# Optimization experiments

Hardware: AMD Instinct MI355X
Metric: run time of the kernel (lower is better)

Reference implementation:

```python
import jax, jax.numpy as jnp
import numpy as np

N = 50000   # total_ent
R = 16      # total_rel
D = 64      # emb_dim
F_IN = 128  # feat_in
L = 2       # gcn_layers
E = 100000  # edges per relation
EPS = 1e-12


def setup_inputs() -> dict:
    key = jax.random.key(0)
    ks = jax.random.split(key, 6)
    x = jax.random.normal(ks[0], (N, F_IN), jnp.float32)
    # xavier-uniform-ish scaled params
    ent_emb = jax.random.normal(ks[1], (F_IN, D), jnp.float32) * (1.0 / np.sqrt(F_IN))
    rel_trans = jax.random.normal(ks[2], (L, R, D, D), jnp.float32) * (1.0 / np.sqrt(D))
    edge_row = jax.random.randint(ks[3], (R, E), 0, N)
    edge_col = jax.random.randint(ks[4], (R, E), 0, N)
    edge_val = jax.random.uniform(ks[5], (R, E), jnp.float32)
    return dict(x=x, ent_emb=ent_emb, rel_trans=rel_trans,
                edge_row=edge_row, edge_col=edge_col, edge_val=edge_val)


def reference(x, ent_emb, rel_trans, edge_row, edge_col, edge_val):
    # emb = x @ ent_emb : [N, D]
    emb = x @ ent_emb

    def spmm_per_rel(emb):
        # per-relation sparse.mm: out[r, row] += val * emb[col]
        def one_rel(row, col, val):
            return jax.ops.segment_sum(val[:, None] * emb[col], row, num_segments=N)
        return jax.vmap(one_rel)(edge_row, edge_col, edge_val)  # [R, N, D]

    for l in range(L):
        emb_acc = spmm_per_rel(emb)                             # [R, N, D]
        # tmp[r] = (W_r @ emb_acc[r]^T)^T = emb_acc[r] @ W_r^T
        tmp = jnp.einsum('rne,rde->rnd', emb_acc, rel_trans[l])  # [R, N, D]
        emb = jax.nn.relu(tmp.sum(axis=0))                       # [N, D]

    # F.normalize(emb) : L2 over dim=1 with eps clamp
    norm = jnp.linalg.norm(emb, axis=1, keepdims=True)
    return emb / jnp.maximum(norm, EPS)
```

## Files before the change

### kernel.cpp

```cpp
#include <hip/hip_runtime.h>

#define Nn 50000
#define Rr 16
#define Dd 64
#define Fin 128
#define Ee 100000
#define NE (Rr * Ee)
#define NBKT 782
#define CB 256
#define EPB (NE / CB)
#define SCTOT (NBKT * CB)
#define SC_NB (SCTOT / 256)
#define NTILE (Nn / 16)

typedef __attribute__((ext_vector_type(8))) short short8;
typedef __attribute__((ext_vector_type(4))) float f32x4;
typedef unsigned short ushort_t;

__device__ inline ushort_t f2bf(float x) {
  union { float f; unsigned u; } v; v.f = x;
  unsigned u = v.u;
  return (ushort_t)((u + 0x7FFFu + ((u >> 16) & 1u)) >> 16);
}
__device__ inline float bf2f(ushort_t h) {
  union { unsigned u; float f; } v; v.u = ((unsigned)h) << 16; return v.f;
}

#define INIT_TILES 3125
#define INIT_NB 782
#define CONVW_NB 512
__global__ __launch_bounds__(256) void pre_k(const float* __restrict__ x,
                                             const float* __restrict__ ent,
                                             ushort_t* __restrict__ emb0,
                                             const float* __restrict__ rel,
                                             ushort_t* __restrict__ wbf,
                                             const int* __restrict__ erow,
                                             int* __restrict__ cnt) {
  __shared__ int lh[NBKT];
  int b = blockIdx.x;
  if (b < INIT_NB) {
    int wave = threadIdx.x >> 6, lane = threadIdx.x & 63;
    int nt = lane & 15, quad = lane >> 4;
    int tile = b * 4 + wave;
    if (tile >= INIT_TILES) return;
    const float* xr = x + ((long)tile * 16 + nt) * Fin + quad * 8;
    short8 afrag[4];
#pragma unroll
    for (int ks = 0; ks < 4; ++ks) {
      float4 p0 = *(const float4*)(xr + ks * 32);
      float4 p1 = *(const float4*)(xr + ks * 32 + 4);
      short8 a;
      a[0] = (short)f2bf(p0.x); a[1] = (short)f2bf(p0.y);
      a[2] = (short)f2bf(p0.z); a[3] = (short)f2bf(p0.w);
      a[4] = (short)f2bf(p1.x); a[5] = (short)f2bf(p1.y);
      a[6] = (short)f2bf(p1.z); a[7] = (short)f2bf(p1.w);
      afrag[ks] = a;
    }
    f32x4 acc[4];
#pragma unroll
    for (int dt = 0; dt < 4; ++dt) acc[dt] = (f32x4){0.f, 0.f, 0.f, 0.f};
#pragma unroll
    for (int ks = 0; ks < 4; ++ks) {
#pragma unroll
      for (int dt = 0; dt < 4; ++dt) {
        short8 bfr;
#pragma unroll
        for (int j = 0; j < 8; ++j)
          bfr[j] = (short)f2bf(ent[(unsigned)(ks * 32 + quad * 8 + j) * Dd + dt * 16 + nt]);
        acc[dt] = __builtin_amdgcn_mfma_f32_16x16x32_bf16(afrag[ks], bfr, acc[dt], 0, 0, 0);
      }
    }
#pragma unroll
    for (int dt = 0; dt < 4; ++dt)
#pragma unroll
      for (int reg = 0; reg < 4; ++reg) {
        int row = tile * 16 + quad * 4 + reg;
        emb0[(unsigned)row * Dd + dt * 16 + nt] = f2bf(acc[dt][reg]);
      }
  } else if (b < INIT_NB + CONVW_NB) {
    int i = (b - INIT_NB) * 256 + threadIdx.x;
    wbf[i] = f2bf(rel[i]);
  } else {
    int blk = b - INIT_NB - CONVW_NB;
    int t = threadIdx.x;
    for (int i = t; i < NBKT; i += 256) lh[i] = 0;
    __syncthreads();
    int r = blk >> 4;
    long gbase = (long)r * Ee + (blk & 15) * EPB;
    for (int i = t; i < EPB; i += 256)
      atomicAdd(&lh[erow[gbase + i] >> 6], 1);
    __syncthreads();
    for (int i = t; i < NBKT; i += 256) cnt[i * CB + blk] = lh[i];
  }
}

__global__ __launch_bounds__(256) void scan1_k(const int* __restrict__ cnt,
                                               int* __restrict__ bsum) {
  __shared__ int ls[256];
  int t = threadIdx.x;
  ls[t] = cnt[blockIdx.x * 256 + t];
  __syncthreads();
  for (int off = 128; off >= 1; off >>= 1) {
    if (t < off) ls[t] += ls[t + off];
    __syncthreads();
  }
  if (t == 0) bsum[blockIdx.x] = ls[0];
}

__global__ __launch_bounds__(1024) void scan2_k(int* __restrict__ bsum) {
  __shared__ int ls[1024];
  int t = threadIdx.x;
  int v = (t < SC_NB) ? bsum[t] : 0;
  ls[t] = v;
  __syncthreads();
  for (int off = 1; off < 1024; off <<= 1) {
    int x = (t >= off) ? ls[t - off] : 0;
    __syncthreads();
    ls[t] += x;
    __syncthreads();
  }
  if (t < SC_NB) bsum[t] = ls[t] - v;
}

__global__ __launch_bounds__(256) void scan3_k(int* __restrict__ cnt,
                                               const int* __restrict__ bsum,
                                               int* __restrict__ cbase,
                                               int* __restrict__ offs) {
  __shared__ int ls[256];
  int t = threadIdx.x, i = blockIdx.x * 256 + t;
  int v = cnt[i];
  ls[t] = v;
  __syncthreads();
  for (int off = 1; off < 256; off <<= 1) {
    int x = (t >= off) ? ls[t - off] : 0;
    __syncthreads();
    ls[t] += x;
    __syncthreads();
  }
  int excl = ls[t] - v + bsum[blockIdx.x];
  cnt[i] = excl;
  if (t == 0) cbase[blockIdx.x] = excl;
  if (i == SCTOT - 1) { cbase[NBKT] = NE; offs[Nn] = NE; }
}

__global__ __launch_bounds__(256) void place_k(const int* __restrict__ erow,
                                               const int* __restrict__ ecol,
                                               const float* __restrict__ ev,
                                               const int* __restrict__ base,
                                               uint2* __restrict__ ebkt) {
  __shared__ int lofs[NBKT];
  int blk = blockIdx.x, t = threadIdx.x;
  for (int i = t; i < NBKT; i += 256) lofs[i] = base[i * CB + blk];
  __syncthreads();
  int r = blk >> 4;
  long gbase = (long)r * Ee + (blk & 15) * EPB;
  for (int i = t; i < EPB; i += 256) {
    long idx = gbase + i;
    int row = erow[idx];
    int pos = atomicAdd(&lofs[row >> 6], 1);
    unsigned vb = f2bf(ev[idx]);
    ebkt[pos] = make_uint2(((unsigned)(row & 63) << 4) | (unsigned)r,
                           (vb << 16) | (unsigned)ecol[idx]);
  }
}

__global__ __launch_bounds__(256) void csort_k(const uint2* __restrict__ ebkt,
                                               const int* __restrict__ cbase,
                                               uint2* __restrict__ ed2,
                                               int* __restrict__ offs) {
  __shared__ int lcnt[64], lstart[64], lcur[64];
  int c = blockIdx.x, t = threadIdx.x;
  int s = cbase[c], e = cbase[c + 1];
  if (t < 64) lcnt[t] = 0;
  __syncthreads();
  for (int i = s + t; i < e; i += 256) atomicAdd(&lcnt[ebkt[i].x >> 4], 1);
  __syncthreads();
  if (t == 0) {
    int run = 0;
    for (int rl = 0; rl < 64; ++rl) {
      int cc = lcnt[rl];
      lstart[rl] = run; lcur[rl] = run; run += cc;
    }
  }
  __syncthreads();
  int nrow = Nn - c * 64; if (nrow > 64) nrow = 64;
  if (t < nrow) offs[c * 64 + t] = s + lstart[t];
  for (int i = s + t; i < e; i += 256) {
    uint2 q = ebkt[i];
    int pos = s + atomicAdd(&lcur[q.x >> 4], 1);
    ed2[pos] = make_uint2(q.x & 15u, q.y);
  }
}

__global__ __launch_bounds__(256) void fused_k(const ushort_t* __restrict__ emb,
                                               const int* __restrict__ offs,
                                               const uint2* __restrict__ ed2,
                                               const ushort_t* __restrict__ wl,
                                               ushort_t* __restrict__ embout,
                                               float* __restrict__ finout,
                                               int fin) {
  __shared__ ushort_t Zt[16 * 1024];
  __shared__ f32x4 ssred[4][4];
  const int lane = threadIdx.x & 63;
  const int wave = threadIdx.x >> 6;
  const int nt = lane & 15, quad = lane >> 4;
  const int tile = blockIdx.x;

  const int qb = quad << 3;
  const ushort_t* embnt = emb + nt;
  char* ztb = (char*)Zt;
  union AW { unsigned w[4]; short8 v; };

  for (int rr = 0; rr < 4; ++rr) {
    const int rl = wave * 4 + rr;
    const int row = tile * 16 + rl;
    int off_l = (lane < 2) ? offs[row + lane] : 0;
    const int base = __shfl(off_l, 0, 64);
    const int len  = __shfl(off_l, 1, 64) - base;

    f32x4 acc[4];
#pragma unroll
    for (int dt = 0; dt < 4; ++dt) acc[dt] = (f32x4){0.f, 0.f, 0.f, 0.f};

    for (int c = 0; c < len; c += 32) {
      int p = c + (lane & 31);
      uint2 myed = (p < len) ? ed2[base + p] : make_uint2(0u, 0u);

      unsigned yw[4][4];
      unsigned aw[4];
#pragma unroll
      for (int jp = 0; jp < 4; ++jp) {
        unsigned q0 = (unsigned)__shfl((int)myed.y, qb + 2 * jp, 64);
        unsigned q1 = (unsigned)__shfl((int)myed.y, qb + 2 * jp + 1, 64);
        unsigned x0 = (unsigned)__shfl((int)myed.x, qb + 2 * jp, 64);
        unsigned x1 = (unsigned)__shfl((int)myed.x, qb + 2 * jp + 1, 64);
        const ushort_t* e0 = embnt + (q0 & 0xFFFFu) * 64u;
        const ushort_t* e1 = embnt + (q1 & 0xFFFFu) * 64u;
#pragma unroll
        for (int dt = 0; dt < 4; ++dt)
          yw[dt][jp] = (unsigned)e0[dt * 16] | ((unsigned)e1[dt * 16] << 16);
        unsigned t0 = (x0 == (unsigned)nt) ? (q0 >> 16) : 0u;
        unsigned t1 = (x1 == (unsigned)nt) ? (q1 >> 16) : 0u;
        aw[jp] = t0 | (t1 << 16);
      }

      AW af;
      af.w[0] = aw[0]; af.w[1] = aw[1]; af.w[2] = aw[2]; af.w[3] = aw[3];
#pragma unroll
      for (int dt = 0; dt < 4; ++dt) {
        AW bf;
#pragma unroll
        for (int jp = 0; jp < 4; ++jp) bf.w[jp] = yw[dt][jp];
        acc[dt] = __builtin_amdgcn_mfma_f32_16x16x32_bf16(af.v, bf.v, acc[dt], 0, 0, 0);
      }
    }

    const unsigned swz = (unsigned)((rl & 7) << 4);
    const unsigned rb = (unsigned)(rl * 2048 + quad * 512);
#pragma unroll
    for (int dt = 0; dt < 4; ++dt)
#pragma unroll
      for (int reg = 0; reg < 4; ++reg) {
        unsigned hv = (unsigned)f2bf(acc[dt][reg]);
        unsigned pv = (unsigned)__shfl_xor((int)hv, 1, 64);
        if ((nt & 1) == 0) {
          unsigned lg = rb + (unsigned)(reg * 128 + dt * 32 + nt * 2);
          *(unsigned*)(ztb + (lg ^ swz)) = hv | (pv << 16);
        }
      }
  }
  __syncthreads();

  const int s0 = nt * 2048 + (((quad    ) ^ (nt & 7)) << 4);
  const int s1 = nt * 2048 + (((quad + 4) ^ (nt & 7)) << 4);
  f32x4 accA = (f32x4){0.f, 0.f, 0.f, 0.f};
  f32x4 accB = (f32x4){0.f, 0.f, 0.f, 0.f};
#pragma unroll
  for (int r = 0; r < 16; r += 2) {
    const char* ab0 = ztb + r * 128;
    const char* ab1 = ztb + (r + 1) * 128;
    short8 a00 = *(const short8*)(ab0 + s0);
    short8 a01 = *(const short8*)(ab0 + s1);
    short8 a10 = *(const short8*)(ab1 + s0);
    short8 a11 = *(const short8*)(ab1 + s1);
    const ushort_t* bp0 = wl + (unsigned)(r * Dd + wave * 16 + nt) * Dd + qb;
    const ushort_t* bp1 = wl + (unsigned)((r + 1) * Dd + wave * 16 + nt) * Dd + qb;
    short8 b00 = *(const short8*)(bp0);
    short8 b01 = *(const short8*)(bp0 + 32);
    short8 b10 = *(const short8*)(bp1);
    short8 b11 = *(const short8*)(bp1 + 32);
    accA = __builtin_amdgcn_mfma_f32_16x16x32_bf16(a00, b00, accA, 0, 0, 0);
    accA = __builtin_amdgcn_mfma_f32_16x16x32_bf16(a01, b01, accA, 0, 0, 0);
    accB = __builtin_amdgcn_mfma_f32_16x16x32_bf16(a10, b10, accB, 0, 0, 0);
    accB = __builtin_amdgcn_mfma_f32_16x16x32_bf16(a11, b11, accB, 0, 0, 0);
  }
  f32x4 accO;
#pragma unroll
  for (int reg = 0; reg < 4; ++reg) accO[reg] = accA[reg] + accB[reg];

  if (!fin) {
#pragma unroll
    for (int reg = 0; reg < 4; ++reg) {
      int row = tile * 16 + quad * 4 + reg;
      embout[(unsigned)row * 64u + wave * 16 + nt] = f2bf(fmaxf(accO[reg], 0.f));
    }
  } else {
    float v[4];
    f32x4 ssq;
#pragma unroll
    for (int reg = 0; reg < 4; ++reg) {
      v[reg] = fmaxf(accO[reg], 0.f);
      ssq[reg] = v[reg] * v[reg];
    }
#pragma unroll
    for (int off = 8; off >= 1; off >>= 1)
#pragma unroll
      for (int reg = 0; reg < 4; ++reg)
        ssq[reg] += __shfl_xor(ssq[reg], off, 64);
    if (nt == 0) ssred[wave][quad] = ssq;
    __syncthreads();
    f32x4 t0 = ssred[0][quad], t1 = ssred[1][quad];
    f32x4 t2 = ssred[2][quad], t3 = ssred[3][quad];
#pragma unroll
    for (int reg = 0; reg < 4; ++reg) {
      float tot = t0[reg] + t1[reg] + t2[reg] + t3[reg];
      float sc = 1.f / fmaxf(sqrtf(tot), 1e-12f);
      int row = tile * 16 + quad * 4 + reg;
      finout[(unsigned)row * 64u + wave * 16 + nt] = v[reg] * sc;
    }
  }
}

extern "C" void kernel_launch(void* const* d_in, const int* in_sizes, int n_in,
                              void* d_out, int out_size, void* d_ws, size_t ws_size,
                              hipStream_t stream) {
  const float* x   = (const float*)d_in[0];
  const float* ent = (const float*)d_in[1];
  const float* rel = (const float*)d_in[2];
  const int* erow  = (const int*)d_in[3];
  const int* ecol  = (const int*)d_in[4];
  const float* ev  = (const float*)d_in[5];
  float* out = (float*)d_out;

  char* p = (char*)d_ws;
  ushort_t* emb_a = (ushort_t*)p;  p += (size_t)Nn * Dd * 2;
  ushort_t* emb_b = (ushort_t*)p;  p += (size_t)Nn * Dd * 2;
  ushort_t* wbf   = (ushort_t*)p;  p += (size_t)2 * Rr * Dd * Dd * 2;
  uint2* ebkt     = (uint2*)p;     p += (size_t)NE * 8;
  uint2* ed2      = (uint2*)p;     p += (size_t)NE * 8;
  int* cnt        = (int*)p;       p += (size_t)SCTOT * 4;
  int* bsum       = (int*)p;       p += (size_t)(SC_NB + 8) * 4;
  int* cbase      = (int*)p;       p += (size_t)(NBKT + 8) * 4;
  int* offs       = (int*)p;       p += (size_t)(Nn + 8) * 4;

  pre_k<<<INIT_NB + CONVW_NB + CB, 256, 0, stream>>>(
      x, ent, emb_a, rel, wbf, erow, cnt);
  scan1_k<<<SC_NB, 256, 0, stream>>>(cnt, bsum);
  scan2_k<<<1, 1024, 0, stream>>>(bsum);
  scan3_k<<<SC_NB, 256, 0, stream>>>(cnt, bsum, cbase, offs);
  place_k<<<CB, 256, 0, stream>>>(erow, ecol, ev, cnt, ebkt);
  csort_k<<<NBKT, 256, 0, stream>>>(ebkt, cbase, ed2, offs);

  fused_k<<<NTILE, 256, 0, stream>>>(emb_a, offs, ed2, wbf, emb_b, nullptr, 0);
  fused_k<<<NTILE, 256, 0, stream>>>(emb_b, offs, ed2,
                                     wbf + (size_t)Rr * Dd * Dd, nullptr, out, 1);
}
```

Measured before the change: 330.2 us.

## Replace two-pass bucketed CSR build with direct per-row histogram and atomic scatter

```diff
diff --git a/kernel.cpp b/kernel.cpp
--- a/kernel.cpp
+++ b/kernel.cpp
@@ -6,12 +6,9 @@
 #define Fin 128
 #define Ee 100000
 #define NE (Rr * Ee)
-#define NBKT 782
-#define CB 256
-#define EPB (NE / CB)
-#define SCTOT (NBKT * CB)
-#define SC_NB (SCTOT / 256)
 #define NTILE (Nn / 16)
+#define NROW_PAD 50176
+#define SCAN_NB 196
 
 typedef __attribute__((ext_vector_type(8))) short short8;
 typedef __attribute__((ext_vector_type(4))) float f32x4;
@@ -29,14 +26,14 @@
 #define INIT_TILES 3125
 #define INIT_NB 782
 #define CONVW_NB 512
+#define HIST_NB 256
 __global__ __launch_bounds__(256) void pre_k(const float* __restrict__ x,
                                              const float* __restrict__ ent,
                                              ushort_t* __restrict__ emb0,
                                              const float* __restrict__ rel,
                                              ushort_t* __restrict__ wbf,
                                              const int* __restrict__ erow,
-                                             int* __restrict__ cnt) {
-  __shared__ int lh[NBKT];
+                                             int* __restrict__ cnt50) {
   int b = blockIdx.x;
   if (b < INIT_NB) {
     int wave = threadIdx.x >> 6, lane = threadIdx.x & 63;
@@ -81,21 +78,14 @@
     int i = (b - INIT_NB) * 256 + threadIdx.x;
     wbf[i] = f2bf(rel[i]);
   } else {
-    int blk = b - INIT_NB - CONVW_NB;
-    int t = threadIdx.x;
-    for (int i = t; i < NBKT; i += 256) lh[i] = 0;
-    __syncthreads();
-    int r = blk >> 4;
-    long gbase = (long)r * Ee + (blk & 15) * EPB;
-    for (int i = t; i < EPB; i += 256)
-      atomicAdd(&lh[erow[gbase + i] >> 6], 1);
-    __syncthreads();
-    for (int i = t; i < NBKT; i += 256) cnt[i * CB + blk] = lh[i];
-  }
-}
-
-__global__ __launch_bounds__(256) void scan1_k(const int* __restrict__ cnt,
-                                               int* __restrict__ bsum) {
+    int t = (b - INIT_NB - CONVW_NB) * 256 + threadIdx.x;
+    for (int i = t; i < NE; i += HIST_NB * 256)
+      atomicAdd(&cnt50[erow[i]], 1);
+  }
+}
+
+__global__ __launch_bounds__(256) void sA1_k(const int* __restrict__ cnt,
+                                             int* __restrict__ bsum) {
   __shared__ int ls[256];
   int t = threadIdx.x;
   ls[t] = cnt[blockIdx.x * 256 + t];
@@ -107,25 +97,25 @@
   if (t == 0) bsum[blockIdx.x] = ls[0];
 }
 
-__global__ __launch_bounds__(1024) void scan2_k(int* __restrict__ bsum) {
-  __shared__ int ls[1024];
+__global__ __launch_bounds__(256) void sA2_k(int* __restrict__ bsum) {
+  __shared__ int ls[256];
   int t = threadIdx.x;
-  int v = (t < SC_NB) ? bsum[t] : 0;
+  int v = (t < SCAN_NB) ? bsum[t] : 0;
   ls[t] = v;
   __syncthreads();
-  for (int off = 1; off < 1024; off <<= 1) {
+  for (int off = 1; off < 256; off <<= 1) {
     int x = (t >= off) ? ls[t - off] : 0;
     __syncthreads();
     ls[t] += x;
     __syncthreads();
   }
-  if (t < SC_NB) bsum[t] = ls[t] - v;
-}
-
-__global__ __launch_bounds__(256) void scan3_k(int* __restrict__ cnt,
-                                               const int* __restrict__ bsum,
-                                               int* __restrict__ cbase,
-                                               int* __restrict__ offs) {
+  if (t < SCAN_NB) bsum[t] = ls[t] - v;
+}
+
+__global__ __launch_bounds__(256) void sA3_k(const int* __restrict__ cnt,
+                                             const int* __restrict__ bsum,
+                                             int* __restrict__ offs,
+                                             int* __restrict__ cur) {
   __shared__ int ls[256];
   int t = threadIdx.x, i = blockIdx.x * 256 + t;
   int v = cnt[i];
@@ -138,58 +128,21 @@
     __syncthreads();
   }
   int excl = ls[t] - v + bsum[blockIdx.x];
-  cnt[i] = excl;
-  if (t == 0) cbase[blockIdx.x] = excl;
-  if (i == SCTOT - 1) { cbase[NBKT] = NE; offs[Nn] = NE; }
-}
-
-__global__ __launch_bounds__(256) void place_k(const int* __restrict__ erow,
-                                               const int* __restrict__ ecol,
-                                               const float* __restrict__ ev,
-                                               const int* __restrict__ base,
-                                               uint2* __restrict__ ebkt) {
-  __shared__ int lofs[NBKT];
-  int blk = blockIdx.x, t = threadIdx.x;
-  for (int i = t; i < NBKT; i += 256) lofs[i] = base[i * CB + blk];
-  __syncthreads();
-  int r = blk >> 4;
-  long gbase = (long)r * Ee + (blk & 15) * EPB;
-  for (int i = t; i < EPB; i += 256) {
-    long idx = gbase + i;
-    int row = erow[idx];
-    int pos = atomicAdd(&lofs[row >> 6], 1);
-    unsigned vb = f2bf(ev[idx]);
-    ebkt[pos] = make_uint2(((unsigned)(row & 63) << 4) | (unsigned)r,
-                           (vb << 16) | (unsigned)ecol[idx]);
-  }
-}
-
-__global__ __launch_bounds__(256) void csort_k(const uint2* __restrict__ ebkt,
-                                               const int* __restrict__ cbase,
-                                               uint2* __restrict__ ed2,
-                                               int* __restrict__ offs) {
-  __shared__ int lcnt[64], lstart[64], lcur[64];
-  int c = blockIdx.x, t = threadIdx.x;
-  int s = cbase[c], e = cbase[c + 1];
-  if (t < 64) lcnt[t] = 0;
-  __syncthreads();
-  for (int i = s + t; i < e; i += 256) atomicAdd(&lcnt[ebkt[i].x >> 4], 1);
-  __syncthreads();
-  if (t == 0) {
-    int run = 0;
-    for (int rl = 0; rl < 64; ++rl) {
-      int cc = lcnt[rl];
-      lstart[rl] = run; lcur[rl] = run; run += cc;
-    }
-  }
-  __syncthreads();
-  int nrow = Nn - c * 64; if (nrow > 64) nrow = 64;
-  if (t < nrow) offs[c * 64 + t] = s + lstart[t];
-  for (int i = s + t; i < e; i += 256) {
-    uint2 q = ebkt[i];
-    int pos = s + atomicAdd(&lcur[q.x >> 4], 1);
-    ed2[pos] = make_uint2(q.x & 15u, q.y);
-  }
+  if (i <= Nn) offs[i] = excl;
+  if (i < Nn) cur[i] = excl;
+}
+
+__global__ __launch_bounds__(256) void place2_k(const int* __restrict__ erow,
+                                                const int* __restrict__ ecol,
+                                                const float* __restrict__ ev,
+                                                int* __restrict__ cur,
+                                                uint2* __restrict__ ed2) {
+  int idx = blockIdx.x * 256 + threadIdx.x;
+  int r = idx / Ee;
+  int row = erow[idx];
+  unsigned vb = f2bf(ev[idx]);
+  int pos = atomicAdd(&cur[row], 1);
+  ed2[pos] = make_uint2((unsigned)r, (vb << 16) | (unsigned)ecol[idx]);
 }
 
 __global__ __launch_bounds__(256) void fused_k(const ushort_t* __restrict__ emb,
@@ -346,20 +299,19 @@
   ushort_t* emb_a = (ushort_t*)p;  p += (size_t)Nn * Dd * 2;
   ushort_t* emb_b = (ushort_t*)p;  p += (size_t)Nn * Dd * 2;
   ushort_t* wbf   = (ushort_t*)p;  p += (size_t)2 * Rr * Dd * Dd * 2;
-  uint2* ebkt     = (uint2*)p;     p += (size_t)NE * 8;
   uint2* ed2      = (uint2*)p;     p += (size_t)NE * 8;
-  int* cnt        = (int*)p;       p += (size_t)SCTOT * 4;
-  int* bsum       = (int*)p;       p += (size_t)(SC_NB + 8) * 4;
-  int* cbase      = (int*)p;       p += (size_t)(NBKT + 8) * 4;
+  int* cnt50      = (int*)p;       p += (size_t)NROW_PAD * 4;
+  int* cur        = (int*)p;       p += (size_t)NROW_PAD * 4;
+  int* bsum       = (int*)p;       p += (size_t)(SCAN_NB + 8) * 4;
   int* offs       = (int*)p;       p += (size_t)(Nn + 8) * 4;
 
-  pre_k<<<INIT_NB + CONVW_NB + CB, 256, 0, stream>>>(
-      x, ent, emb_a, rel, wbf, erow, cnt);
-  scan1_k<<<SC_NB, 256, 0, stream>>>(cnt, bsum);
-  scan2_k<<<1, 1024, 0, stream>>>(bsum);
-  scan3_k<<<SC_NB, 256, 0, stream>>>(cnt, bsum, cbase, offs);
-  place_k<<<CB, 256, 0, stream>>>(erow, ecol, ev, cnt, ebkt);
-  csort_k<<<NBKT, 256, 0, stream>>>(ebkt, cbase, ed2, offs);
+  hipMemsetAsync(cnt50, 0, (size_t)NROW_PAD * 4, stream);
+  pre_k<<<INIT_NB + CONVW_NB + HIST_NB, 256, 0, stream>>>(
+      x, ent, emb_a, rel, wbf, erow, cnt50);
+  sA1_k<<<SCAN_NB, 256, 0, stream>>>(cnt50, bsum);
+  sA2_k<<<1, 256, 0, stream>>>(bsum);
+  sA3_k<<<SCAN_NB, 256, 0, stream>>>(cnt50, bsum, offs, cur);
+  place2_k<<<NE / 256, 256, 0, stream>>>(erow, ecol, ev, cur, ed2);
 
   fused_k<<<NTILE, 256, 0, stream>>>(emb_a, offs, ed2, wbf, emb_b, nullptr, 0);
   fused_k<<<NTILE, 256, 0, stream>>>(emb_b, offs, ed2,
```

Result: slower. 466.5 us (+41.3%).
